# Performance work log

Measured on AMD Instinct MI355X. Metric: run time of the kernel, lower is better.

Reference implementation:

```python
import jax, jax.numpy as jnp
import numpy as np

MUL_IN = 128      # multiplicity of each input irrep (0e,1e,2e)
MUL_H = 16        # hidden multiplicity per irrep in MLP_irreps
N_NODES = 100000
D_IN = MUL_IN * (1 + 3 + 5)  # 1152


def setup_inputs() -> dict:
    key = jax.random.key(0)
    ks = jax.random.split(key, 7)
    x = jax.random.normal(ks[0], (N_NODES, D_IN), dtype=jnp.float32)
    # linear_1: 128x0e+128x1e+128x2e -> 48x0e + 16x1e + 16x2e (scalars+gates = 16+32 = 48 0e)
    w1_0 = jax.random.normal(ks[1], (MUL_IN, 3 * MUL_H), dtype=jnp.float32)  # [128,48]
    w1_1 = jax.random.normal(ks[2], (MUL_IN, MUL_H), dtype=jnp.float32)      # [128,16]
    w1_2 = jax.random.normal(ks[3], (MUL_IN, MUL_H), dtype=jnp.float32)      # [128,16]
    # linear_2: 16x0e+16x1e+16x2e -> 1x0e+1x1e+1x2e
    w2_0 = jax.random.normal(ks[4], (MUL_H, 1), dtype=jnp.float32)
    w2_1 = jax.random.normal(ks[5], (MUL_H, 1), dtype=jnp.float32)
    w2_2 = jax.random.normal(ks[6], (MUL_H, 1), dtype=jnp.float32)
    return {"x": x, "w1_0": w1_0, "w1_1": w1_1, "w1_2": w1_2,
            "w2_0": w2_0, "w2_1": w2_1, "w2_2": w2_2}


def reference(x, w1_0, w1_1, w1_2, w2_0, w2_1, w2_2):
    n = x.shape[0]
    inv_in = 1.0 / np.sqrt(MUL_IN).astype(np.float32)
    inv_h = 1.0 / np.sqrt(MUL_H).astype(np.float32)
    # split input into irreps: 0e [n,128], 1e [n,128,3], 2e [n,128,5]
    x0 = x[:, :MUL_IN]
    x1 = x[:, MUL_IN:MUL_IN + 3 * MUL_IN].reshape(n, MUL_IN, 3)
    x2 = x[:, MUL_IN + 3 * MUL_IN:].reshape(n, MUL_IN, 5)
    # linear_1 (per-irrep GEMM over multiplicity, e3nn path norm 1/sqrt(fan_in))
    y0 = (x0 @ w1_0) * inv_in                               # [n,48] = scalars(16) + gates(32)
    y1 = jnp.einsum('nui,uv->nvi', x1, w1_1) * inv_in        # [n,16,3]
    y2 = jnp.einsum('nui,uv->nvi', x2, w1_2) * inv_in        # [n,16,5]
    # Gate: silu on scalars and gates, multiply gates into gated irreps
    s = jax.nn.silu(y0[:, :MUL_H])                           # [n,16] scalars 0e
    g = jax.nn.silu(y0[:, MUL_H:])                           # [n,32] gates
    z1 = y1 * g[:, :MUL_H, None]                             # [n,16,3]
    z2 = y2 * g[:, MUL_H:, None]                             # [n,16,5]
    # linear_2 -> 1x0e + 1x1e + 1x2e
    o0 = (s @ w2_0) * inv_h                                  # [n,1]
    o1 = jnp.einsum('nui,uv->nvi', z1, w2_1) * inv_h         # [n,1,3]
    o2 = jnp.einsum('nui,uv->nvi', z2, w2_2) * inv_h         # [n,1,5]
    return jnp.concatenate([o0, o1.reshape(n, 3), o2.reshape(n, 5)], axis=1)  # [n,9]
```

## Files before the change

### kernel.cpp

```cpp
#include <hip/hip_runtime.h>

#define NN   100000
#define DIN  1152


__global__ void __launch_bounds__(256) prep_weights(
    const float* __restrict__ w10, const float* __restrict__ w11,
    const float* __restrict__ w12, const float* __restrict__ w20,
    const float* __restrict__ w21, const float* __restrict__ w22,
    float* __restrict__ ws) {
  int t = blockIdx.x * 256 + threadIdx.x;
  const float inv_in = 0.08838834764831845f;
  const float inv_ih = 0.25f * 0.08838834764831845f;
  if (t < 6144) ws[t] = w10[t] * inv_in;
  if (t < 2048) {
    int v = t & 15;
    ws[6144 + t] = w11[t] * w21[v] * inv_ih;
    ws[8192 + t] = w12[t] * w22[v] * inv_ih;
  }
  if (t < 16) ws[10240 + t] = w20[t] * 0.25f;
}

__global__ void __launch_bounds__(256) fused_node_kernel(
    const float* __restrict__ x, const float* __restrict__ ws,
    float* __restrict__ out) {
  const int node = blockIdx.x * 256 + threadIdx.x;
  if (node >= NN) return;

  const float* __restrict__ W0  = ws;
  const float* __restrict__ W1  = ws + 6144;
  const float* __restrict__ W2  = ws + 8192;
  const float* __restrict__ W20 = ws + 10240;
  const float4* __restrict__ xr =
      reinterpret_cast<const float4*>(x + (size_t)node * DIN);

  float y0[48];
  #pragma unroll
  for (int v = 0; v < 48; ++v) y0[v] = 0.f;

  #pragma unroll 2
  for (int q = 0; q < 32; ++q) {
    float4 d = xr[q];
    const float* w = W0 + q * 192;
    #pragma unroll
    for (int v = 0; v < 48; ++v)
      y0[v] = fmaf(d.x, w[v],
              fmaf(d.y, w[48 + v],
              fmaf(d.z, w[96 + v],
              fmaf(d.w, w[144 + v], y0[v]))));
  }

  float o0 = 0.f;
  float g1[16], g2[16];
  #pragma unroll
  for (int v = 0; v < 16; ++v) {
    float t = y0[v];
    o0 = fmaf(t / (1.f + __expf(-t)), W20[v], o0);
  }
  #pragma unroll
  for (int v = 0; v < 16; ++v) { float t = y0[16 + v]; g1[v] = t / (1.f + __expf(-t)); }
  #pragma unroll
  for (int v = 0; v < 16; ++v) { float t = y0[32 + v]; g2[v] = t / (1.f + __expf(-t)); }

  float o1[3] = {0.f, 0.f, 0.f};
  #pragma unroll 2
  for (int k = 0; k < 32; ++k) {
    float4 a = xr[32 + 3 * k], b = xr[33 + 3 * k], c = xr[34 + 3 * k];
    float e[12] = {a.x, a.y, a.z, a.w, b.x, b.y, b.z, b.w, c.x, c.y, c.z, c.w};
    #pragma unroll
    for (int j = 0; j < 4; ++j) {
      const float* wp = W1 + (4 * k + j) * 16;
      float tmp = 0.f;
      #pragma unroll
      for (int v = 0; v < 16; ++v) tmp = fmaf(wp[v], g1[v], tmp);
      #pragma unroll
      for (int i = 0; i < 3; ++i) o1[i] = fmaf(e[3 * j + i], tmp, o1[i]);
    }
  }

  float o2[5] = {0.f, 0.f, 0.f, 0.f, 0.f};
  #pragma unroll 2
  for (int k = 0; k < 32; ++k) {
    float4 a = xr[128 + 5 * k], b = xr[129 + 5 * k], c = xr[130 + 5 * k],
           d = xr[131 + 5 * k], f = xr[132 + 5 * k];
    float e[20] = {a.x, a.y, a.z, a.w, b.x, b.y, b.z, b.w, c.x, c.y, c.z, c.w,
                   d.x, d.y, d.z, d.w, f.x, f.y, f.z, f.w};
    #pragma unroll
    for (int j = 0; j < 4; ++j) {
      const float* wp = W2 + (4 * k + j) * 16;
      float tmp = 0.f;
      #pragma unroll
      for (int v = 0; v < 16; ++v) tmp = fmaf(wp[v], g2[v], tmp);
      #pragma unroll
      for (int i = 0; i < 5; ++i) o2[i] = fmaf(e[5 * j + i], tmp, o2[i]);
    }
  }

  float* po = out + (size_t)node * 9;
  po[0] = o0;
  #pragma unroll
  for (int i = 0; i < 3; ++i) po[1 + i] = o1[i];
  #pragma unroll
  for (int i = 0; i < 5; ++i) po[4 + i] = o2[i];
}

extern "C" void kernel_launch(void* const* d_in, const int* in_sizes, int n_in,
                              void* d_out, int out_size, void* d_ws, size_t ws_size,
                              hipStream_t stream) {
  const float* x   = (const float*)d_in[0];
  const float* w10 = (const float*)d_in[1];
  const float* w11 = (const float*)d_in[2];
  const float* w12 = (const float*)d_in[3];
  const float* w20 = (const float*)d_in[4];
  const float* w21 = (const float*)d_in[5];
  const float* w22 = (const float*)d_in[6];
  float* ws = (float*)d_ws;

  prep_weights<<<24, 256, 0, stream>>>(w10, w11, w12, w20, w21, w22, ws);

  int blocks = (NN + 255) / 256;
  fused_node_kernel<<<blocks, 256, 0, stream>>>(x, ws, (float*)d_out);
}
```

Baseline: 654.5 us.

## Split each node's reduction across four waves with shared-memory partial sums

Each block now handles 64 nodes, and its four wavefronts each take a quarter of the input multiplicity for the first linear layer and the gated second stage. Partial sums are combined through shared memory with several block barriers, and wave 0 computes the gates and broadcasts them. The aim is more waves per node, so more parallelism and memory-level concurrency over the long per-thread serial loops. The cost is extra LDS traffic, barriers, and a lower occupancy hint through launch_bounds(256,4).

```diff
diff --git a/kernel.cpp b/kernel.cpp
--- a/kernel.cpp
+++ b/kernel.cpp
@@ -21,87 +21,158 @@
   if (t < 16) ws[10240 + t] = w20[t] * 0.25f;
 }
 
-__global__ void __launch_bounds__(256) fused_node_kernel(
+__device__ __forceinline__ float silu(float t) {
+  return t / (1.f + __expf(-t));
+}
+
+__global__ void __launch_bounds__(256, 4) fused_node_kernel(
     const float* __restrict__ x, const float* __restrict__ ws,
     float* __restrict__ out) {
-  const int node = blockIdx.x * 256 + threadIdx.x;
-  if (node >= NN) return;
+  __shared__ float smem[6272];
+  float* red0 = smem;
+  float* red1 = smem + 3136;
+  float* gbuf = smem;
+  float* obuf = smem + 3136;
+
+  const int lane = threadIdx.x & 63;
+  const int w    = threadIdx.x >> 6;
+  const int nb   = blockIdx.x * 64;
+  const int node = nb + lane;
+  const int nrow = node < NN ? node : NN - 1;
+  const float4* __restrict__ xr =
+      reinterpret_cast<const float4*>(x + (size_t)nrow * DIN);
 
   const float* __restrict__ W0  = ws;
   const float* __restrict__ W1  = ws + 6144;
   const float* __restrict__ W2  = ws + 8192;
   const float* __restrict__ W20 = ws + 10240;
-  const float4* __restrict__ xr =
-      reinterpret_cast<const float4*>(x + (size_t)node * DIN);
 
-  float y0[48];
+  float y0p[48];
   #pragma unroll
-  for (int v = 0; v < 48; ++v) y0[v] = 0.f;
-
-  #pragma unroll 2
-  for (int q = 0; q < 32; ++q) {
-    float4 d = xr[q];
-    const float* w = W0 + q * 192;
+  for (int v = 0; v < 48; ++v) y0p[v] = 0.f;
+  {
+    const float* Wb = W0 + (32 * w) * 48;
     #pragma unroll
-    for (int v = 0; v < 48; ++v)
-      y0[v] = fmaf(d.x, w[v],
-              fmaf(d.y, w[48 + v],
-              fmaf(d.z, w[96 + v],
-              fmaf(d.w, w[144 + v], y0[v]))));
-  }
-
-  float o0 = 0.f;
-  float g1[16], g2[16];
-  #pragma unroll
-  for (int v = 0; v < 16; ++v) {
-    float t = y0[v];
-    o0 = fmaf(t / (1.f + __expf(-t)), W20[v], o0);
-  }
-  #pragma unroll
-  for (int v = 0; v < 16; ++v) { float t = y0[16 + v]; g1[v] = t / (1.f + __expf(-t)); }
-  #pragma unroll
-  for (int v = 0; v < 16; ++v) { float t = y0[32 + v]; g2[v] = t / (1.f + __expf(-t)); }
-
-  float o1[3] = {0.f, 0.f, 0.f};
-  #pragma unroll 2
-  for (int k = 0; k < 32; ++k) {
-    float4 a = xr[32 + 3 * k], b = xr[33 + 3 * k], c = xr[34 + 3 * k];
-    float e[12] = {a.x, a.y, a.z, a.w, b.x, b.y, b.z, b.w, c.x, c.y, c.z, c.w};
-    #pragma unroll
-    for (int j = 0; j < 4; ++j) {
-      const float* wp = W1 + (4 * k + j) * 16;
-      float tmp = 0.f;
+    for (int q = 0; q < 8; ++q) {
+      float4 d = xr[8 * w + q];
+      const float* wp = Wb + q * 192;
       #pragma unroll
-      for (int v = 0; v < 16; ++v) tmp = fmaf(wp[v], g1[v], tmp);
-      #pragma unroll
-      for (int i = 0; i < 3; ++i) o1[i] = fmaf(e[3 * j + i], tmp, o1[i]);
+      for (int v = 0; v < 48; ++v)
+        y0p[v] = fmaf(d.x, wp[v],
+                 fmaf(d.y, wp[48 + v],
+                 fmaf(d.z, wp[96 + v],
+                 fmaf(d.w, wp[144 + v], y0p[v]))));
     }
   }
 
-  float o2[5] = {0.f, 0.f, 0.f, 0.f, 0.f};
-  #pragma unroll 2
-  for (int k = 0; k < 32; ++k) {
-    float4 a = xr[128 + 5 * k], b = xr[129 + 5 * k], c = xr[130 + 5 * k],
-           d = xr[131 + 5 * k], f = xr[132 + 5 * k];
-    float e[20] = {a.x, a.y, a.z, a.w, b.x, b.y, b.z, b.w, c.x, c.y, c.z, c.w,
-                   d.x, d.y, d.z, d.w, f.x, f.y, f.z, f.w};
+  if (w >= 2) {
+    float* dst = (w == 2 ? red0 : red1) + lane * 49;
     #pragma unroll
-    for (int j = 0; j < 4; ++j) {
-      const float* wp = W2 + (4 * k + j) * 16;
-      float tmp = 0.f;
+    for (int v = 0; v < 48; ++v) dst[v] = y0p[v];
+  }
+  __syncthreads();
+  if (w == 0) {
+    const float* b = red0 + lane * 49;
+    #pragma unroll
+    for (int v = 0; v < 48; ++v) y0p[v] += b[v];
+  } else if (w == 1) {
+    float* b = red1 + lane * 49;
+    #pragma unroll
+    for (int v = 0; v < 48; ++v) { y0p[v] += b[v]; b[v] = y0p[v]; }
+  }
+  __syncthreads();
+
+  float g1[16], g2[16];
+  float o0 = 0.f;
+  if (w == 0) {
+    const float* b = red1 + lane * 49;
+    #pragma unroll
+    for (int v = 0; v < 48; ++v) y0p[v] += b[v];
+    #pragma unroll
+    for (int v = 0; v < 16; ++v) o0 = fmaf(silu(y0p[v]), W20[v], o0);
+    #pragma unroll
+    for (int v = 0; v < 16; ++v) g1[v] = silu(y0p[16 + v]);
+    #pragma unroll
+    for (int v = 0; v < 16; ++v) g2[v] = silu(y0p[32 + v]);
+    float* gp = gbuf + lane * 33;
+    #pragma unroll
+    for (int v = 0; v < 16; ++v) { gp[v] = g1[v]; gp[16 + v] = g2[v]; }
+  }
+  __syncthreads();
+  if (w != 0) {
+    const float* gp = gbuf + lane * 33;
+    #pragma unroll
+    for (int v = 0; v < 16; ++v) { g1[v] = gp[v]; g2[v] = gp[16 + v]; }
+  }
+
+  float o1p[3] = {0.f, 0.f, 0.f};
+  {
+    float t1[32];
+    const float* Wb = W1 + (32 * w) * 16;
+    #pragma unroll
+    for (int uu = 0; uu < 32; ++uu) {
+      float s = 0.f;
       #pragma unroll
-      for (int v = 0; v < 16; ++v) tmp = fmaf(wp[v], g2[v], tmp);
-      #pragma unroll
-      for (int i = 0; i < 5; ++i) o2[i] = fmaf(e[5 * j + i], tmp, o2[i]);
+      for (int v = 0; v < 16; ++v) s = fmaf(Wb[uu * 16 + v], g1[v], s);
+      t1[uu] = s;
+    }
+    const float4* p = xr + 32 + 24 * w;
+    #pragma unroll
+    for (int k = 0; k < 24; ++k) {
+      float4 d = p[k];
+      o1p[(4 * k + 0) % 3] = fmaf(d.x, t1[(4 * k + 0) / 3], o1p[(4 * k + 0) % 3]);
+      o1p[(4 * k + 1) % 3] = fmaf(d.y, t1[(4 * k + 1) / 3], o1p[(4 * k + 1) % 3]);
+      o1p[(4 * k + 2) % 3] = fmaf(d.z, t1[(4 * k + 2) / 3], o1p[(4 * k + 2) % 3]);
+      o1p[(4 * k + 3) % 3] = fmaf(d.w, t1[(4 * k + 3) / 3], o1p[(4 * k + 3) % 3]);
     }
   }
 
-  float* po = out + (size_t)node * 9;
-  po[0] = o0;
-  #pragma unroll
-  for (int i = 0; i < 3; ++i) po[1 + i] = o1[i];
-  #pragma unroll
-  for (int i = 0; i < 5; ++i) po[4 + i] = o2[i];
+  float o2p[5] = {0.f, 0.f, 0.f, 0.f, 0.f};
+  {
+    float t2[32];
+    const float* Wb = W2 + (32 * w) * 16;
+    #pragma unroll
+    for (int uu = 0; uu < 32; ++uu) {
+      float s = 0.f;
+      #pragma unroll
+      for (int v = 0; v < 16; ++v) s = fmaf(Wb[uu * 16 + v], g2[v], s);
+      t2[uu] = s;
+    }
+    const float4* p = xr + 128 + 40 * w;
+    #pragma unroll
+    for (int k = 0; k < 40; ++k) {
+      float4 d = p[k];
+      o2p[(4 * k + 0) % 5] = fmaf(d.x, t2[(4 * k + 0) / 5], o2p[(4 * k + 0) % 5]);
+      o2p[(4 * k + 1) % 5] = fmaf(d.y, t2[(4 * k + 1) / 5], o2p[(4 * k + 1) % 5]);
+      o2p[(4 * k + 2) % 5] = fmaf(d.z, t2[(4 * k + 2) / 5], o2p[(4 * k + 2) % 5]);
+      o2p[(4 * k + 3) % 5] = fmaf(d.w, t2[(4 * k + 3) / 5], o2p[(4 * k + 3) % 5]);
+    }
+  }
+
+  if (w != 0) {
+    float* op = obuf + (w - 1) * 576 + lane * 9;
+    #pragma unroll
+    for (int i = 0; i < 3; ++i) op[i] = o1p[i];
+    #pragma unroll
+    for (int i = 0; i < 5; ++i) op[3 + i] = o2p[i];
+  }
+  __syncthreads();
+  if (w == 0 && node < NN) {
+    #pragma unroll
+    for (int wi = 0; wi < 3; ++wi) {
+      const float* op = obuf + wi * 576 + lane * 9;
+      #pragma unroll
+      for (int i = 0; i < 3; ++i) o1p[i] += op[i];
+      #pragma unroll
+      for (int i = 0; i < 5; ++i) o2p[i] += op[3 + i];
+    }
+    float* po = out + (size_t)node * 9;
+    po[0] = o0;
+    #pragma unroll
+    for (int i = 0; i < 3; ++i) po[1 + i] = o1p[i];
+    #pragma unroll
+    for (int i = 0; i < 5; ++i) po[4 + i] = o2p[i];
+  }
 }
 
 extern "C" void kernel_launch(void* const* d_in, const int* in_sizes, int n_in,
@@ -118,6 +189,6 @@
 
   prep_weights<<<24, 256, 0, stream>>>(w10, w11, w12, w20, w21, w22, ws);
 
-  int blocks = (NN + 255) / 256;
+  int blocks = (NN + 63) / 64;
   fused_node_kernel<<<blocks, 256, 0, stream>>>(x, ws, (float*)d_out);
 }
```

Result: slower. 799.2 us (+22.1%).
